# Kernel tuning notes

Measured on AMD Instinct MI355X. Metric: run time of the kernel, lower is better.

## Reference

```python
import jax, jax.numpy as jnp
import numpy as np
import math

B, S, D, H = 2, 2048, 1024, 16
HD = D // H  # 64 head features


def setup_inputs() -> dict:
    key = jax.random.key(0)
    ks = jax.random.split(key, 6)
    x = jax.random.normal(ks[0], (B, S, D), jnp.float32)
    wq = jax.random.normal(ks[1], (D, D), jnp.float32) * 0.02
    wk = jax.random.normal(ks[2], (D, D), jnp.float32) * 0.02
    wv = jax.random.normal(ks[3], (D, D), jnp.float32) * 0.02
    wo = jax.random.normal(ks[4], (D, D), jnp.float32) * 0.02
    # Llama-style RoPE frequencies: unit-modulus complex per (pos, pair),
    # stored as separate cos/sin arrays of shape [S, HD//2].
    inv_freq = 1.0 / (10000.0 ** (jnp.arange(0, HD, 2, dtype=jnp.float32) / HD))
    ang = jnp.arange(S, dtype=jnp.float32)[:, None] * inv_freq[None, :]
    freq_cos = jnp.cos(ang)
    freq_sin = jnp.sin(ang)
    # realistic padding: each sequence keeps a random prefix of at least S//2 tokens
    lengths = jax.random.randint(ks[5], (B,), S // 2, S + 1)
    padding_mask = (jnp.arange(S)[None, :] < lengths[:, None]).astype(jnp.int32)
    return dict(x=x, wq=wq, wk=wk, wv=wv, wo=wo,
                freq_cos=freq_cos, freq_sin=freq_sin, padding_mask=padding_mask)


def _apply_rope(t, cos, sin):
    # t: [B, S, H, HD]; cos/sin: [S, HD//2]
    tr = t.reshape(t.shape[:-1] + (HD // 2, 2))
    t0, t1 = tr[..., 0], tr[..., 1]
    c = cos[None, :, None, :]
    s = sin[None, :, None, :]
    o0 = t0 * c - t1 * s  # real part of complex multiply
    o1 = t0 * s + t1 * c  # imag part
    return jnp.stack([o0, o1], axis=-1).reshape(t.shape)


def reference(x, wq, wk, wv, wo, freq_cos, freq_sin, padding_mask):
    # QKV projections (torch Linear: y = x @ W.T, no bias)
    q = (x @ wq.T).reshape(B, S, H, HD)
    k = (x @ wk.T).reshape(B, S, H, HD)
    v = (x @ wv.T).reshape(B, S, H, HD)
    q = _apply_rope(q, freq_cos, freq_sin)
    k = _apply_rope(k, freq_cos, freq_sin)
    q = jnp.transpose(q, (0, 2, 1, 3))  # [B,H,S,HD]
    k = jnp.transpose(k, (0, 2, 1, 3))
    v = jnp.transpose(v, (0, 2, 1, 3))
    # NOTE: original scales by sqrt(n_features), not sqrt(head_dim)
    scores = jnp.einsum('bhqd,bhkd->bhqk', q, k) / math.sqrt(D)
    bias = jnp.where(padding_mask[:, None, None, :] == 0,
                     jnp.float32(-jnp.inf), jnp.float32(0.0))
    p = jax.nn.softmax(scores + bias, axis=-1)
    out = jnp.einsum('bhqk,bhkd->bhqd', p, v)
    out = jnp.transpose(out, (0, 2, 1, 3)).reshape(B, S, D)
    return out @ wo.T
```

## Files before the change

kernel.cpp:

```cpp
#include <hip/hip_runtime.h>
#include <hip/hip_bf16.h>
#include <stdint.h>

typedef unsigned short u16;
typedef __attribute__((ext_vector_type(8))) short bf16x8;
typedef __attribute__((ext_vector_type(4))) float f32x4;
typedef __attribute__((ext_vector_type(16))) float f32x16;

__device__ __forceinline__ u16 f2bf(float f) {
  union { float f; uint32_t u; } a; a.f = f;
  return (u16)((a.u + 0x7FFFu + ((a.u >> 16) & 1u)) >> 16);
}

__device__ __forceinline__ void gload_lds16(const void* g, void* l) {
  auto* gp = (__attribute__((address_space(1))) void*)(uintptr_t)g;
  auto* lp = (__attribute__((address_space(3))) void*)(uintptr_t)l;
  __builtin_amdgcn_global_load_lds(gp, lp, 16, 0, 0);
}

__device__ __forceinline__ float exp2_fast(float x) {
  float r;
  asm("v_exp_f32 %0, %1" : "=v"(r) : "v"(x));
  return r;
}

template <int N> __device__ __forceinline__ void waitvm() {
  if constexpr (N == 3)      asm volatile("s_waitcnt vmcnt(3)" ::: "memory");
  else if constexpr (N == 4) asm volatile("s_waitcnt vmcnt(4)" ::: "memory");
  else                       asm volatile("s_waitcnt vmcnt(0)" ::: "memory");
}

#define CVTPK(d, a, b) asm("v_cvt_pk_bf16_f32 %0, %1, %2" : "=v"(d) : "v"(a), "v"(b))
#define SWAP32(a, b)   asm("v_permlane32_swap_b32 %0, %1" : "+v"(a), "+v"(b))
#define BARRIER() do { asm volatile("" ::: "memory"); __builtin_amdgcn_s_barrier(); asm volatile("" ::: "memory"); } while (0)
#define WAITVM0() asm volatile("s_waitcnt vmcnt(0)" ::: "memory")

__global__ void cvt_kernel(const float4* __restrict__ x, const float4* __restrict__ wq,
                           const float4* __restrict__ wk, const float4* __restrict__ wv,
                           const float4* __restrict__ wo,
                           ushort4* __restrict__ xb, ushort4* __restrict__ wqkv,
                           ushort4* __restrict__ wob,
                           const int* __restrict__ mask, int* __restrict__ lens) {
  if (blockIdx.x >= 2048) {
    __shared__ int red[256];
    int b = blockIdx.x - 2048, s = 0;
    for (int i = threadIdx.x; i < 2048; i += 256) s += mask[b * 2048 + i];
    red[threadIdx.x] = s;
    __syncthreads();
    if (threadIdx.x < 64) {
      int v = red[threadIdx.x] + red[threadIdx.x + 64] + red[threadIdx.x + 128] + red[threadIdx.x + 192];
      #pragma unroll
      for (int o = 32; o > 0; o >>= 1) v += __shfl_down(v, o);
      if (threadIdx.x == 0) lens[b] = v;
    }
    return;
  }
  const int XN = (2 * 2048 * 1024) / 4;
  const int WN = (1024 * 1024) / 4;
  const int total = XN + 4 * WN;
  for (int i = blockIdx.x * 256 + threadIdx.x; i < total; i += 2048 * 256) {
    float4 v; ushort4* dst;
    if (i < XN) { v = x[i]; dst = xb + i; }
    else {
      int j = i - XN; int m = j >> 18; int o = j & (WN - 1);
      const float4* src = (m == 0) ? wq : (m == 1) ? wk : (m == 2) ? wv : wo;
      v = src[o];
      dst = (m < 3) ? (wqkv + j) : (wob + o);
    }
    ushort4 r; r.x = f2bf(v.x); r.y = f2bf(v.y); r.z = f2bf(v.z); r.w = f2bf(v.w);
    *dst = r;
  }
}

__global__ __launch_bounds__(512, 1)
void gemm2ph(const u16* __restrict__ A, const u16* __restrict__ Bm, int nTm,
             u16* __restrict__ Qb, u16* __restrict__ Kb, u16* __restrict__ VbT,
             const float* __restrict__ cosT, const float* __restrict__ sinT) {
  extern __shared__ __align__(16) u16 lds[];
  u16* SA = lds;
  u16* SB = lds + 32768;
  const int tid = threadIdx.x, lane = tid & 63, wid = tid >> 6;
  const int wm = (wid >> 2) * 128, wn = (wid & 3) * 64;
  const int lr = lane & 15, lg = lane >> 4;

  const int cpx = gridDim.x >> 3;
  const int bid = (blockIdx.x & 7) * cpx + (blockIdx.x >> 3);
  const int m0 = (bid % nTm) * 256;
  const int n0 = (bid / nTm) * 256;

  const int srow = tid >> 3;
  const int schunk = (tid & 7) ^ ((srow >> 1) & 7);
  const u16* gA = A + (int64_t)(m0 + srow) * 1024 + schunk * 8;
  const u16* gB = Bm + (int64_t)(n0 + srow) * 1024 + schunk * 8;
  const int sdst = wid * 512;

#define STG(buf, t) do { const int _ko = (t) * 64; \
    _Pragma("unroll") for (int j = 0; j < 4; ++j) \
      gload_lds16(gA + (int64_t)(j * 64) * 1024 + _ko, &SA[(buf) * 16384 + j * 4096 + sdst]); \
    _Pragma("unroll") for (int j = 0; j < 4; ++j) \
      gload_lds16(gB + (int64_t)(j * 64) * 1024 + _ko, &SB[(buf) * 16384 + j * 4096 + sdst]); } while (0)

  f32x4 acc[8][4];
  #pragma unroll
  for (int i = 0; i < 8; ++i)
    #pragma unroll
    for (int j = 0; j < 4; ++j)
      #pragma unroll
      for (int e = 0; e < 4; ++e) acc[i][j][e] = 0.0f;

  STG(0, 0);
  WAITVM0();
  BARRIER();

  for (int t = 0; t < 16; ++t) {
    const int bu = t & 1;
    if (t < 15) STG(bu ^ 1, t + 1);
    const u16* sa = &SA[bu * 16384];
    const u16* sb = &SB[bu * 16384];
    #pragma unroll
    for (int ks = 0; ks < 2; ++ks) {
      bf16x8 af[8], bfm[4];
      #pragma unroll
      for (int mi = 0; mi < 8; ++mi) {
        const int row = wm + mi * 16 + lr;
        af[mi] = *(const bf16x8*)&sa[row * 64 + (((ks * 4 + lg) ^ ((row >> 1) & 7)) * 8)];
      }
      #pragma unroll
      for (int ni = 0; ni < 4; ++ni) {
        const int row = wn + ni * 16 + lr;
        bfm[ni] = *(const bf16x8*)&sb[row * 64 + (((ks * 4 + lg) ^ ((row >> 1) & 7)) * 8)];
      }
      __builtin_amdgcn_s_setprio(1);
      #pragma unroll
      for (int mi = 0; mi < 8; ++mi)
        #pragma unroll
        for (int ni = 0; ni < 4; ++ni)
          acc[mi][ni] = __builtin_amdgcn_mfma_f32_16x16x32_bf16(af[mi], bfm[ni], acc[mi][ni], 0, 0, 0);
      __builtin_amdgcn_s_setprio(0);
    }
    WAITVM0();
    BARRIER();
  }

  #pragma unroll
  for (int mi = 0; mi < 8; ++mi) {
    #pragma unroll
    for (int r = 0; r < 4; ++r) {
      const int row = m0 + wm + mi * 16 + lg * 4 + r;
      const int bb = row >> 11, ss = row & 2047;
      #pragma unroll
      for (int ni = 0; ni < 4; ++ni) {
        const int n = n0 + wn + ni * 16 + lr;
        float v = acc[mi][ni][r];
        if (n < 2048) {
          float partner = __shfl_xor(v, 1);
          const int ii = (n >> 1) & 31;
          const float c = cosT[ss * 32 + ii];
          const float sn = sinT[ss * 32 + ii];
          float rv = (n & 1) ? (partner * sn + v * c) : (v * c - partner * sn);
          const int h = (n >> 6) & 15, d = n & 63;
          const int idx = ((bb * 16 + h) * 2048 + ss) * 64 + d;
          if (n < 1024) Qb[idx] = f2bf(rv * 0.0450842298f);
          else          Kb[idx] = f2bf(rv);
        } else {
          const int n2 = n - 2048;
          const int h = n2 >> 6, d = n2 & 63;
          VbT[((int64_t)(bb * 16 + h) * 64 + d) * 2048 + ss] = f2bf(v);
        }
      }
    }
  }
#undef STG
}

template <int BM, int BN, int MODE>
__global__ __launch_bounds__(256, 3)
void gemm3(const u16* __restrict__ A, const u16* __restrict__ Bm,
           int nTm, float* __restrict__ outf,
           u16* __restrict__ Qb, u16* __restrict__ Kb, u16* __restrict__ VbT,
           const float* __restrict__ cosT, const float* __restrict__ sinT) {
  constexpr int MREP = BM / 32;
  constexpr int NREP = BN / 32;
  constexpr int LA = BM / 64;
  constexpr int LB = BN / 64;
  constexpr int LOADS = LA + LB;
  __shared__ alignas(16) u16 SA[3][BM * 32];
  __shared__ alignas(16) u16 SB[3][BN * 32];

  const int tid = threadIdx.x, lane = tid & 63, wid = tid >> 6;
  const int wm = (wid >> 1) * (BM / 2), wn = (wid & 1) * (BN / 2);
  const int lr = lane & 15, lg = lane >> 4;

  const int cpx = gridDim.x >> 3;
  const int bid = (blockIdx.x & 7) * cpx + (blockIdx.x >> 3);
  const int m0 = (bid % nTm) * BM;
  const int n0 = (bid / nTm) * BN;

  const int srow = tid >> 2;
  const int schunk = (tid & 3) ^ ((srow >> 1) & 3);
  const u16* gA = A + (int64_t)(m0 + srow) * 1024 + schunk * 8;
  const u16* gB = Bm + (int64_t)(n0 + srow) * 1024 + schunk * 8;
  const int sdst = wid * 512;

#define STAGE(b, t) do { const int _ko = (t) * 32; \
    _Pragma("unroll") for (int j = 0; j < LA; ++j) \
      gload_lds16(gA + (int64_t)(j * 64) * 1024 + _ko, &SA[b][j * 2048 + sdst]); \
    _Pragma("unroll") for (int j = 0; j < LB; ++j) \
      gload_lds16(gB + (int64_t)(j * 64) * 1024 + _ko, &SB[b][j * 2048 + sdst]); } while (0)

  f32x4 acc[MREP][NREP];
  #pragma unroll
  for (int i = 0; i < MREP; ++i)
    #pragma unroll
    for (int j = 0; j < NREP; ++j)
      #pragma unroll
      for (int e = 0; e < 4; ++e) acc[i][j][e] = 0.0f;

  const int rchunk = (lg ^ ((lr >> 1) & 3)) * 8;

  STAGE(0, 0);
  STAGE(1, 1);
  waitvm<LOADS>();
  BARRIER();

  int bc = 0, bs = 2;
  for (int t = 0; t < 32; ++t) {
    if (t < 30) STAGE(bs, t + 2);
    const u16* sa = SA[bc];
    const u16* sb = SB[bc];
    bf16x8 af[MREP], bfm[NREP];
    #pragma unroll
    for (int i = 0; i < MREP; ++i) af[i] = *(const bf16x8*)&sa[(wm + i * 16 + lr) * 32 + rchunk];
    #pragma unroll
    for (int i = 0; i < NREP; ++i) bfm[i] = *(const bf16x8*)&sb[(wn + i * 16 + lr) * 32 + rchunk];
    #pragma unroll
    for (int mi = 0; mi < MREP; ++mi)
      #pragma unroll
      for (int ni = 0; ni < NREP; ++ni)
        acc[mi][ni] = __builtin_amdgcn_mfma_f32_16x16x32_bf16(af[mi], bfm[ni], acc[mi][ni], 0, 0, 0);
    if (t < 30) waitvm<LOADS>();
    else        waitvm<0>();
    BARRIER();
    bc = (bc == 2) ? 0 : bc + 1;
    bs = (bs == 2) ? 0 : bs + 1;
  }

  if (MODE == 0) {
    #pragma unroll
    for (int mi = 0; mi < MREP; ++mi)
      #pragma unroll
      for (int r = 0; r < 4; ++r) {
        const int row = m0 + wm + mi * 16 + lg * 4 + r;
        float* orow = outf + (int64_t)row * 1024 + n0 + wn + lr;
        #pragma unroll
        for (int ni = 0; ni < NREP; ++ni) orow[ni * 16] = acc[mi][ni][r];
      }
  }
#undef STAGE
}

__global__ __launch_bounds__(256, 2)
void attn_kernel(const u16* __restrict__ Qb, const u16* __restrict__ Kb,
                 const u16* __restrict__ VbT, u16* __restrict__ attnb,
                 const int* __restrict__ lens) {
  __shared__ alignas(16) u16 Klds[2][2][64 * 64];
  __shared__ alignas(16) u16 Vlds[2][2][64 * 64];
  const int tid = threadIdx.x, lane = tid & 63, wid = tid >> 6;
  const int hi = lane >> 5, ql = lane & 31;
  const int bh = blockIdx.x >> 4;
  const int len = lens[bh >> 4];
  const int qrow = (blockIdx.x & 15) * 128 + wid * 32 + ql;

  bf16x8 qf[4];
  const u16* qptr = Qb + ((int64_t)bh * 2048 + qrow) * 64 + hi * 8;
  #pragma unroll
  for (int c = 0; c < 4; ++c) qf[c] = *(const bf16x8*)(qptr + c * 16);

  const int srow = tid >> 3, schunk = (tid & 7) ^ (srow & 7);
  const u16* kg = Kb + ((int64_t)bh * 2048 + srow) * 64 + schunk * 8;
  const u16* vg = VbT + ((int64_t)bh * 64 + srow) * 2048 + schunk * 8;
  const int dstoff = wid * 512;

#define ASTAGE(b, t) do { const int _k0 = (t) * 128; \
    _Pragma("unroll") for (int su = 0; su < 2; ++su) { \
      gload_lds16(kg + (int64_t)(_k0 + su * 64) * 64,        &Klds[b][su][dstoff]); \
      gload_lds16(kg + (int64_t)(_k0 + su * 64 + 32) * 64,   &Klds[b][su][2048 + dstoff]); \
      gload_lds16(vg + _k0 + su * 64,                        &Vlds[b][su][dstoff]); \
      gload_lds16(vg + _k0 + su * 64 + 32 * 2048,            &Vlds[b][su][2048 + dstoff]); } } while (0)

  f32x16 oacc[2];
  #pragma unroll
  for (int r = 0; r < 16; ++r) { oacc[0][r] = 0.0f; oacc[1][r] = 0.0f; }
  float mrun = -1e30f, lrun = 0.0f;

  const int nt = (len + 127) >> 7;
  ASTAGE(0, 0);
  __syncthreads();

  for (int t = 0; t < nt; ++t) {
    const int bu = t & 1;
    if (t + 1 < nt) ASTAGE(bu ^ 1, t + 1);

    f32x16 s[2][2];
    #pragma unroll
    for (int su = 0; su < 2; ++su)
      #pragma unroll
      for (int h = 0; h < 2; ++h)
        #pragma unroll
        for (int r = 0; r < 16; ++r) s[su][h][r] = 0.0f;
    __builtin_amdgcn_s_setprio(1);
    #pragma unroll
    for (int su = 0; su < 2; ++su)
      #pragma unroll
      for (int c = 0; c < 4; ++c) {
        const int slot = (((2 * c + hi) ^ (ql & 7)) * 8);
        bf16x8 kf0 = *(const bf16x8*)&Klds[bu][su][ql * 64 + slot];
        bf16x8 kf1 = *(const bf16x8*)&Klds[bu][su][(32 + ql) * 64 + slot];
        s[su][0] = __builtin_amdgcn_mfma_f32_32x32x16_bf16(kf0, qf[c], s[su][0], 0, 0, 0);
        s[su][1] = __builtin_amdgcn_mfma_f32_32x32x16_bf16(kf1, qf[c], s[su][1], 0, 0, 0);
      }
    __builtin_amdgcn_s_setprio(0);

    const int k0 = t * 128;
    if (k0 + 128 > len) {
      #pragma unroll
      for (int su = 0; su < 2; ++su)
        #pragma unroll
        for (int r = 0; r < 16; ++r) {
          const int key = k0 + su * 64 + (r & 3) + 8 * (r >> 2) + 4 * hi;
          if (key >= len)      s[su][0][r] = -1e30f;
          if (key + 32 >= len) s[su][1][r] = -1e30f;
        }
    }

    float ma = -1e30f, mb = -1e30f, mc = -1e30f, md = -1e30f;
    #pragma unroll
    for (int su = 0; su < 2; ++su)
      #pragma unroll
      for (int h = 0; h < 2; ++h)
        #pragma unroll
        for (int r = 0; r < 16; r += 4) {
          ma = fmaxf(ma, s[su][h][r]);
          mb = fmaxf(mb, s[su][h][r + 1]);
          mc = fmaxf(mc, s[su][h][r + 2]);
          md = fmaxf(md, s[su][h][r + 3]);
        }
    float mx = fmaxf(fmaxf(ma, mb), fmaxf(mc, md));
    mx = fmaxf(mx, __shfl_xor(mx, 32));
    if (!__all(mx - mrun <= 11.0f)) {
      const float mnew = fmaxf(mrun, mx);
      const float sc = exp2_fast(mrun - mnew);
      #pragma unroll
      for (int r = 0; r < 16; ++r) { oacc[0][r] *= sc; oacc[1][r] *= sc; }
      lrun *= sc;
      mrun = mnew;
    }

    float ps0 = 0.0f, ps1 = 0.0f;
    bf16x8 pfrag[8];
    #pragma unroll
    for (int su = 0; su < 2; ++su) {
      float p0[16], p1[16];
      #pragma unroll
      for (int r = 0; r < 16; r += 2) {
        p0[r]     = exp2_fast(s[su][0][r] - mrun);
        p0[r + 1] = exp2_fast(s[su][0][r + 1] - mrun);
        p1[r]     = exp2_fast(s[su][1][r] - mrun);
        p1[r + 1] = exp2_fast(s[su][1][r + 1] - mrun);
        ps0 += p0[r] + p1[r];
        ps1 += p0[r + 1] + p1[r + 1];
      }
      #pragma unroll
      for (int ks = 0; ks < 4; ++ks) {
        const float* pp = (ks < 2) ? p0 : p1;
        const int o = (ks & 1) * 8;
        uint32_t a0, a1, a2, a3;
        CVTPK(a0, pp[o + 0], pp[o + 1]);
        CVTPK(a1, pp[o + 2], pp[o + 3]);
        CVTPK(a2, pp[o + 4], pp[o + 5]);
        CVTPK(a3, pp[o + 6], pp[o + 7]);
        SWAP32(a0, a2);
        SWAP32(a1, a3);
        union { uint32_t u[4]; bf16x8 v; } pw;
        pw.u[0] = a0; pw.u[1] = a1; pw.u[2] = a2; pw.u[3] = a3;
        pfrag[su * 4 + ks] = pw.v;
      }
    }
    float psum = ps0 + ps1;
    psum += __shfl_xor(psum, 32);
    lrun += psum;

    __builtin_amdgcn_s_setprio(1);
    #pragma unroll
    for (int dc = 0; dc < 2; ++dc) {
      const int drow = dc * 32 + ql;
      #pragma unroll
      for (int su = 0; su < 2; ++su)
        #pragma unroll
        for (int ks = 0; ks < 4; ++ks) {
          const int slot = (((2 * ks + hi) ^ (ql & 7)) * 8);
          bf16x8 vf = *(const bf16x8*)&Vlds[bu][su][drow * 64 + slot];
          oacc[dc] = __builtin_amdgcn_mfma_f32_32x32x16_bf16(vf, pfrag[su * 4 + ks], oacc[dc], 0, 0, 0);
        }
    }
    __builtin_amdgcn_s_setprio(0);
    __syncthreads();
  }
#undef ASTAGE

  const float inv = 1.0f / lrun;
  u16* outp = attnb + ((int64_t)((bh >> 4) * 2048 + qrow)) * 1024 + (bh & 15) * 64;
  #pragma unroll
  for (int dc = 0; dc < 2; ++dc)
    #pragma unroll
    for (int g = 0; g < 4; ++g) {
      ushort4 w;
      w.x = f2bf(oacc[dc][4 * g + 0] * inv);
      w.y = f2bf(oacc[dc][4 * g + 1] * inv);
      w.z = f2bf(oacc[dc][4 * g + 2] * inv);
      w.w = f2bf(oacc[dc][4 * g + 3] * inv);
      *(ushort4*)(outp + dc * 32 + 8 * g + 4 * hi) = w;
    }
}

extern "C" void kernel_launch(void* const* d_in, const int* in_sizes, int n_in,
                              void* d_out, int out_size, void* d_ws, size_t ws_size,
                              hipStream_t stream) {
  const float* x    = (const float*)d_in[0];
  const float* wq   = (const float*)d_in[1];
  const float* wk   = (const float*)d_in[2];
  const float* wv   = (const float*)d_in[3];
  const float* wo   = (const float*)d_in[4];
  const float* fcos = (const float*)d_in[5];
  const float* fsin = (const float*)d_in[6];
  const int*   pmsk = (const int*)d_in[7];
  float* out = (float*)d_out;

  char* ws = (char*)d_ws;
  u16* XB    = (u16*)(ws);
  u16* WQKV  = (u16*)(ws + (size_t)8  * 1048576);
  u16* WOB   = (u16*)(ws + (size_t)14 * 1048576);
  u16* QB    = (u16*)(ws + (size_t)16 * 1048576);
  u16* KB    = (u16*)(ws + (size_t)24 * 1048576);
  u16* VBT   = (u16*)(ws + (size_t)32 * 1048576);
  u16* ATTNB = (u16*)(ws + (size_t)40 * 1048576);
  int* LENS  = (int*)(ws + (size_t)48 * 1048576);

  hipFuncSetAttribute((const void*)gemm2ph,
                      hipFuncAttributeMaxDynamicSharedMemorySize, 131072);

  cvt_kernel<<<2050, 256, 0, stream>>>((const float4*)x, (const float4*)wq,
                                       (const float4*)wk, (const float4*)wv,
                                       (const float4*)wo, (ushort4*)XB,
                                       (ushort4*)WQKV, (ushort4*)WOB, pmsk, LENS);

  gemm2ph<<<192, 512, 131072, stream>>>(XB, WQKV, 16, QB, KB, VBT, fcos, fsin);

  attn_kernel<<<512, 256, 0, stream>>>(QB, KB, VBT, ATTNB, LENS);

  gemm3<128, 64, 0><<<512, 256, 0, stream>>>(ATTNB, WOB, 32, out,
                                             nullptr, nullptr, nullptr, nullptr, nullptr);
}
```

Baseline: 122.9 us.

## Replace large-tile QKV GEMM with smaller 128x64 tiles at higher occupancy

Result: slower. 128.3 us (+4.4%).

```diff
diff --git a/kernel.cpp b/kernel.cpp
--- a/kernel.cpp
+++ b/kernel.cpp
@@ -72,105 +72,116 @@
   }
 }
 
-__global__ __launch_bounds__(512, 1)
-void gemm2ph(const u16* __restrict__ A, const u16* __restrict__ Bm, int nTm,
-             u16* __restrict__ Qb, u16* __restrict__ Kb, u16* __restrict__ VbT,
-             const float* __restrict__ cosT, const float* __restrict__ sinT) {
-  extern __shared__ __align__(16) u16 lds[];
-  u16* SA = lds;
-  u16* SB = lds + 32768;
+template <int BM, int BN, int MODE>
+__global__ __launch_bounds__(256, 4)
+void gemm2b(const u16* __restrict__ A, const u16* __restrict__ Bm,
+            int nTm, float* __restrict__ outf,
+            u16* __restrict__ Qb, u16* __restrict__ Kb, u16* __restrict__ VbT,
+            const float* __restrict__ cosT, const float* __restrict__ sinT) {
+  constexpr int MREP = BM / 32;
+  constexpr int NREP = BN / 32;
+  constexpr int LA = BM / 64;
+  constexpr int LB = BN / 64;
+  __shared__ alignas(16) u16 SA[2][BM * 32];
+  __shared__ alignas(16) u16 SB[2][BN * 32];
+
   const int tid = threadIdx.x, lane = tid & 63, wid = tid >> 6;
-  const int wm = (wid >> 2) * 128, wn = (wid & 3) * 64;
+  const int wm = (wid >> 1) * (BM / 2), wn = (wid & 1) * (BN / 2);
   const int lr = lane & 15, lg = lane >> 4;
 
   const int cpx = gridDim.x >> 3;
   const int bid = (blockIdx.x & 7) * cpx + (blockIdx.x >> 3);
-  const int m0 = (bid % nTm) * 256;
-  const int n0 = (bid / nTm) * 256;
-
-  const int srow = tid >> 3;
-  const int schunk = (tid & 7) ^ ((srow >> 1) & 7);
+  const int m0 = (bid % nTm) * BM;
+  const int n0 = (bid / nTm) * BN;
+
+  const int srow = tid >> 2;
+  const int schunk = (tid & 3) ^ ((srow >> 1) & 3);
   const u16* gA = A + (int64_t)(m0 + srow) * 1024 + schunk * 8;
   const u16* gB = Bm + (int64_t)(n0 + srow) * 1024 + schunk * 8;
   const int sdst = wid * 512;
 
-#define STG(buf, t) do { const int _ko = (t) * 64; \
-    _Pragma("unroll") for (int j = 0; j < 4; ++j) \
-      gload_lds16(gA + (int64_t)(j * 64) * 1024 + _ko, &SA[(buf) * 16384 + j * 4096 + sdst]); \
-    _Pragma("unroll") for (int j = 0; j < 4; ++j) \
-      gload_lds16(gB + (int64_t)(j * 64) * 1024 + _ko, &SB[(buf) * 16384 + j * 4096 + sdst]); } while (0)
-
-  f32x4 acc[8][4];
+#define STAGE(b, t) do { const int _ko = (t) * 32; \
+    _Pragma("unroll") for (int j = 0; j < LA; ++j) \
+      gload_lds16(gA + (int64_t)(j * 64) * 1024 + _ko, &SA[b][j * 2048 + sdst]); \
+    _Pragma("unroll") for (int j = 0; j < LB; ++j) \
+      gload_lds16(gB + (int64_t)(j * 64) * 1024 + _ko, &SB[b][j * 2048 + sdst]); } while (0)
+
+  f32x4 acc[MREP][NREP];
   #pragma unroll
-  for (int i = 0; i < 8; ++i)
-    #pragma unroll
-    for (int j = 0; j < 4; ++j)
+  for (int i = 0; i < MREP; ++i)
+    #pragma unroll
+    for (int j = 0; j < NREP; ++j)
       #pragma unroll
       for (int e = 0; e < 4; ++e) acc[i][j][e] = 0.0f;
 
-  STG(0, 0);
+  const int rchunk = (lg ^ ((lr >> 1) & 3)) * 8;
+
+  STAGE(0, 0);
   WAITVM0();
   BARRIER();
 
-  for (int t = 0; t < 16; ++t) {
+  for (int t = 0; t < 32; ++t) {
     const int bu = t & 1;
-    if (t < 15) STG(bu ^ 1, t + 1);
-    const u16* sa = &SA[bu * 16384];
-    const u16* sb = &SB[bu * 16384];
-    #pragma unroll
-    for (int ks = 0; ks < 2; ++ks) {
-      bf16x8 af[8], bfm[4];
-      #pragma unroll
-      for (int mi = 0; mi < 8; ++mi) {
-        const int row = wm + mi * 16 + lr;
-        af[mi] = *(const bf16x8*)&sa[row * 64 + (((ks * 4 + lg) ^ ((row >> 1) & 7)) * 8)];
-      }
-      #pragma unroll
-      for (int ni = 0; ni < 4; ++ni) {
-        const int row = wn + ni * 16 + lr;
-        bfm[ni] = *(const bf16x8*)&sb[row * 64 + (((ks * 4 + lg) ^ ((row >> 1) & 7)) * 8)];
-      }
-      __builtin_amdgcn_s_setprio(1);
-      #pragma unroll
-      for (int mi = 0; mi < 8; ++mi)
-        #pragma unroll
-        for (int ni = 0; ni < 4; ++ni)
-          acc[mi][ni] = __builtin_amdgcn_mfma_f32_16x16x32_bf16(af[mi], bfm[ni], acc[mi][ni], 0, 0, 0);
-      __builtin_amdgcn_s_setprio(0);
-    }
+    if (t < 31) STAGE(bu ^ 1, t + 1);
+    const u16* sa = SA[bu];
+    const u16* sb = SB[bu];
+    bf16x8 af[MREP], bfm[NREP];
+    #pragma unroll
+    for (int i = 0; i < MREP; ++i) af[i] = *(const bf16x8*)&sa[(wm + i * 16 + lr) * 32 + rchunk];
+    #pragma unroll
+    for (int i = 0; i < NREP; ++i) bfm[i] = *(const bf16x8*)&sb[(wn + i * 16 + lr) * 32 + rchunk];
+    __builtin_amdgcn_s_setprio(1);
+    #pragma unroll
+    for (int mi = 0; mi < MREP; ++mi)
+      #pragma unroll
+      for (int ni = 0; ni < NREP; ++ni)
+        acc[mi][ni] = __builtin_amdgcn_mfma_f32_16x16x32_bf16(af[mi], bfm[ni], acc[mi][ni], 0, 0, 0);
+    __builtin_amdgcn_s_setprio(0);
     WAITVM0();
     BARRIER();
   }
 
-  #pragma unroll
-  for (int mi = 0; mi < 8; ++mi) {
-    #pragma unroll
-    for (int r = 0; r < 4; ++r) {
-      const int row = m0 + wm + mi * 16 + lg * 4 + r;
-      const int bb = row >> 11, ss = row & 2047;
-      #pragma unroll
-      for (int ni = 0; ni < 4; ++ni) {
-        const int n = n0 + wn + ni * 16 + lr;
-        float v = acc[mi][ni][r];
-        if (n < 2048) {
-          float partner = __shfl_xor(v, 1);
-          const int ii = (n >> 1) & 31;
-          const float c = cosT[ss * 32 + ii];
-          const float sn = sinT[ss * 32 + ii];
-          float rv = (n & 1) ? (partner * sn + v * c) : (v * c - partner * sn);
-          const int h = (n >> 6) & 15, d = n & 63;
-          const int idx = ((bb * 16 + h) * 2048 + ss) * 64 + d;
-          if (n < 1024) Qb[idx] = f2bf(rv * 0.0450842298f);
-          else          Kb[idx] = f2bf(rv);
-        } else {
-          const int n2 = n - 2048;
-          const int h = n2 >> 6, d = n2 & 63;
-          VbT[((int64_t)(bb * 16 + h) * 64 + d) * 2048 + ss] = f2bf(v);
+  if (MODE == 0) {
+    #pragma unroll
+    for (int mi = 0; mi < MREP; ++mi)
+      #pragma unroll
+      for (int r = 0; r < 4; ++r) {
+        const int row = m0 + wm + mi * 16 + lg * 4 + r;
+        float* orow = outf + (int64_t)row * 1024 + n0 + wn + lr;
+        #pragma unroll
+        for (int ni = 0; ni < NREP; ++ni) orow[ni * 16] = acc[mi][ni][r];
+      }
+  } else {
+    #pragma unroll
+    for (int mi = 0; mi < MREP; ++mi) {
+      #pragma unroll
+      for (int r = 0; r < 4; ++r) {
+        const int row = m0 + wm + mi * 16 + lg * 4 + r;
+        const int bb = row >> 11, ss = row & 2047;
+        #pragma unroll
+        for (int ni = 0; ni < NREP; ++ni) {
+          const int n = n0 + wn + ni * 16 + lr;
+          float v = acc[mi][ni][r];
+          if (n < 2048) {
+            float partner = __shfl_xor(v, 1);
+            const int ii = (n >> 1) & 31;
+            const float c = cosT[ss * 32 + ii];
+            const float sn = sinT[ss * 32 + ii];
+            float rv = (n & 1) ? (partner * sn + v * c) : (v * c - partner * sn);
+            const int h = (n >> 6) & 15, d = n & 63;
+            const int idx = ((bb * 16 + h) * 2048 + ss) * 64 + d;
+            if (n < 1024) Qb[idx] = f2bf(rv * 0.0450842298f);
+            else          Kb[idx] = f2bf(rv);
+          } else {
+            const int n2 = n - 2048;
+            const int h = n2 >> 6, d = n2 & 63;
+            VbT[((int64_t)(bb * 16 + h) * 64 + d) * 2048 + ss] = f2bf(v);
+          }
         }
       }
     }
   }
-#undef STG
+#undef STAGE
 }
 
 template <int BM, int BN, int MODE>
@@ -446,15 +457,13 @@
   u16* ATTNB = (u16*)(ws + (size_t)40 * 1048576);
   int* LENS  = (int*)(ws + (size_t)48 * 1048576);
 
-  hipFuncSetAttribute((const void*)gemm2ph,
-                      hipFuncAttributeMaxDynamicSharedMemorySize, 131072);
-
   cvt_kernel<<<2050, 256, 0, stream>>>((const float4*)x, (const float4*)wq,
                                        (const float4*)wk, (const float4*)wv,
                                        (const float4*)wo, (ushort4*)XB,
                                        (ushort4*)WQKV, (ushort4*)WOB, pmsk, LENS);
 
-  gemm2ph<<<192, 512, 131072, stream>>>(XB, WQKV, 16, QB, KB, VBT, fcos, fsin);
+  gemm2b<128, 64, 1><<<1536, 256, 0, stream>>>(XB, WQKV, 32, nullptr,
+                                               QB, KB, VBT, fcos, fsin);
 
   attn_kernel<<<512, 256, 0, stream>>>(QB, KB, VBT, ATTNB, LENS);
 
```
